# Kernel tuning notes

Measured on AMD Instinct MI355X. Metric: run time of the kernel, lower is better.

Reference implementation:

```python
import jax, jax.numpy as jnp
import numpy as np

B, S, D = 4, 2048, 512

def setup_inputs() -> dict:
    key = jax.random.key(0)
    ks = jax.random.split(key, 7)
    # scale weights so unscaled logits stay in a sane softmax range
    w_scale = 0.05
    return {
        "x": jax.random.normal(ks[0], (B, S, D), dtype=jnp.float32),
        "W_q": jax.random.normal(ks[1], (D, D), dtype=jnp.float32) * w_scale,
        "W_k": jax.random.normal(ks[2], (D, D), dtype=jnp.float32) * w_scale,
        "W_v": jax.random.normal(ks[3], (D, D), dtype=jnp.float32) * w_scale,
        "b_q": jax.random.normal(ks[4], (D,), dtype=jnp.float32) * w_scale,
        "b_k": jax.random.normal(ks[5], (D,), dtype=jnp.float32) * w_scale,
        "b_v": jax.random.normal(ks[6], (D,), dtype=jnp.float32) * w_scale,
    }

def reference(x, W_q, W_k, W_v, b_q, b_k, b_v):
    # QKV projections: [B,S,D] @ [D,D] + [D]
    q = jnp.einsum('bsd,de->bse', x, W_q) + b_q
    k = jnp.einsum('bsd,de->bse', x, W_k) + b_k
    v = jnp.einsum('bsd,de->bse', x, W_v) + b_v
    # unscaled attention scores [B,S,S]
    scores = jnp.einsum('bqd,bkd->bqk', q, k)
    attn = jax.nn.softmax(scores, axis=-1)
    # weighted sum of values [B,S,D]
    return jnp.einsum('bqk,bkd->bqd', attn, v)
```

## Files before the change

### kernel.cpp

```cpp
#include <hip/hip_runtime.h>
#include <hip/hip_bf16.h>
#include <hip/hip_fp16.h>

#define BB 4
#define SS 2048
#define DD 512

typedef short s16x8 __attribute__((ext_vector_type(8)));
typedef short s16x4 __attribute__((ext_vector_type(4)));
typedef float f32x4 __attribute__((ext_vector_type(4)));
typedef _Float16 f16x8 __attribute__((ext_vector_type(8)));

__device__ __forceinline__ short f2h(float f) {
    const _Float16 h = (_Float16)f;
    union { _Float16 h; short s; } u; u.h = h; return u.s;
}
__device__ __forceinline__ float h2f(short s) {
    union { short s; _Float16 h; } u; u.s = s; return (float)u.h;
}
__device__ __forceinline__ f16x8 as_h(s16x8 v) {
    union { s16x8 s; f16x8 h; } u; u.s = v; return u.h;
}

__device__ __forceinline__ void gload_lds16(const void* g, void* l) {
    __builtin_amdgcn_global_load_lds(
        (const __attribute__((address_space(1))) void*)g,
        (__attribute__((address_space(3))) void*)l, 16, 0, 0);
}

#define SB0 __builtin_amdgcn_sched_barrier(0)
#define LGKM0 asm volatile("s_waitcnt lgkmcnt(0)" ::: "memory")
#define VM0   asm volatile("s_waitcnt vmcnt(0)" ::: "memory")

__global__ __launch_bounds__(512, 2) void qkt256(
    const short* __restrict__ qf, const short* __restrict__ kf,
    short* __restrict__ outS, int nwg)
{
    __shared__ short lds[65536];

    const int tid = threadIdx.x;
    const int wave = tid >> 6, lane = tid & 63;
    const int flat = blockIdx.x + 8 * blockIdx.y + 64 * blockIdx.z;
    const int w = (flat & 7) * (nwg >> 3) + (flat >> 3);
    const int bm = ((w >> 3) & 7) * 256, bn = (w & 7) * 256;
    const long z = w >> 6;
    qf += z * (long)SS * DD; kf += z * (long)SS * DD;
    outS += z * (long)SS * SS;

    const int wm = (wave >> 2) * 128, wn = (wave & 3) * 64;
    const int lrow = lane & 15, lk16 = (lane >> 4) * 16;

    f32x4 acc[8][4] = {};

    auto base = [&](int buf, int arr) -> short* { return &lds[(buf * 2 + arr) * 8192]; };
    auto issue = [&](int buf, int arr, int k0) {
#pragma unroll
        for (int h = 0; h < 2; h++) {
            const int Lb = (h << 13) + (tid << 4);
            const int Ls = Lb ^ (((Lb >> 7) & 3) << 4);
            const int row = Ls >> 6, elem = (Ls & 63) >> 1;
            const short* s = arr ? kf : qf;
            const int rb = arr ? bn : bm;
            gload_lds16(s + (size_t)(rb + row) * DD + k0 + elem,
                        (char*)base(buf, arr) + Lb);
        }
    };
    auto rd = [&](int buf, int arr, int row) -> s16x8 {
        const int L = (row << 6) + lk16;
        const int Ls = L ^ (((L >> 7) & 3) << 4);
        return *(const s16x8*)((const char*)base(buf, arr) + Ls);
    };

#define QK_TILE(T, CUR, PREF)                                                    \
  {                                                                              \
    s16x8 a[8], b[4];                                                            \
    _Pragma("unroll")                                                            \
    for (int m = 0; m < 8; m++) a[m] = rd(CUR, 0, wm + m * 16 + lrow);           \
    _Pragma("unroll")                                                            \
    for (int n = 0; n < 4; n++) b[n] = rd(CUR, 1, wn + n * 16 + lrow);           \
    if (PREF) { issue((CUR) ^ 1, 1, ((T) + 1) * 32); SB0;                        \
                issue((CUR) ^ 1, 0, ((T) + 1) * 32); }                           \
    LGKM0; SB0;                                                                  \
    __builtin_amdgcn_s_setprio(1);                                               \
    _Pragma("unroll")                                                            \
    for (int m = 0; m < 8; m++) {                                                \
      _Pragma("unroll")                                                          \
      for (int n = 0; n < 4; n++)                                                \
        acc[m][n] = __builtin_amdgcn_mfma_f32_16x16x32_f16(                      \
            as_h(a[m]), as_h(b[n]), acc[m][n], 0, 0, 0);                         \
    }                                                                            \
    __builtin_amdgcn_s_setprio(0);                                               \
    if (PREF) { VM0; SB0; }                                                      \
    __builtin_amdgcn_s_barrier();                                                \
  }

    issue(0, 1, 0); issue(0, 0, 0);
    VM0;
    __builtin_amdgcn_s_barrier();

    for (int t = 0; t < 16; t += 2) {
        QK_TILE(t,     0, 1);
        QK_TILE(t + 1, 1, (t + 1) < 15);
    }
#undef QK_TILE

    __syncthreads();
    short* ebuf = &lds[0];
#pragma unroll
    for (int m = 0; m < 8; m++) {
#pragma unroll
        for (int n = 0; n < 4; n++) {
#pragma unroll
            for (int j = 0; j < 4; j++) {
                const int rl = wm + m * 16 + (lane >> 4) * 4 + j;
                const int cl = wn + n * 16 + lrow;
                const int pcb = (cl >> 3) ^ ((rl & 3) << 1);
                ebuf[rl * 256 + pcb * 8 + (cl & 7)] =
                    (short)__float2int_rn(acc[m][n][j] * 128.0f);
            }
        }
    }
    __syncthreads();
#pragma unroll
    for (int it = 0; it < 16; it++) {
        const int u = it * 512 + tid;
        const int R = u >> 5, cb = u & 31;
        const int pcb = cb ^ ((R & 3) << 1);
        const s16x8 val = *(const s16x8*)&ebuf[R * 256 + pcb * 8];
        *(s16x8*)&outS[(size_t)(bm + R) * SS + bn + cb * 8] = val;
    }
}

__global__ __launch_bounds__(256, 3) void proj_all(
    const short* __restrict__ xh, const short* __restrict__ xl,
    const short* __restrict__ wt,
    const float* __restrict__ bq, const float* __restrict__ bk,
    const float* __restrict__ bv,
    short* __restrict__ qfp, short* __restrict__ kfp, short* __restrict__ vt)
{
    __shared__ short lds[24576];

    const int tid = threadIdx.x;
    const int wave = tid >> 6, lane = tid & 63;
    const int flat = blockIdx.x + 12 * blockIdx.y;
    const int w = (flat & 7) * 96 + (flat >> 3);
    const int bxi = w % 12, byi = w / 12;
    const int wsel = bxi >> 2;
    const int bnl = (bxi & 3) * 128;
    const int bm = byi * 128;
    const bool lo = (wsel < 2);
    const short* B0 = wt + (size_t)wsel * DD * DD;
    const float* bias = (wsel == 0) ? bq : (wsel == 1) ? bk : bv;

    f32x4 acc[4][4] = {};
    const int wm = (wave >> 1) * 64, wn = (wave & 1) * 64;
    const int lrow = lane & 15, lk16 = (lane >> 4) * 16;

    auto base = [&](int buf, int arr) -> short* { return &lds[(buf * 3 + arr) * 4096]; };
    auto issue = [&](int buf, int arr, int k0) {
#pragma unroll
        for (int h = 0; h < 2; h++) {
            const int Lb = (h << 12) + (tid << 4);
            const int Ls = Lb ^ (((Lb >> 7) & 3) << 4);
            const int row = Ls >> 6, elem = (Ls & 63) >> 1;
            const short* s = (arr == 0) ? xh : (arr == 1) ? xl : B0;
            const int rb = (arr < 2) ? bm : bnl;
            gload_lds16(s + (size_t)(rb + row) * DD + k0 + elem,
                        (char*)base(buf, arr) + Lb);
        }
    };
    auto rd = [&](int buf, int arr, int row) -> s16x8 {
        const int L = (row << 6) + lk16;
        const int Ls = L ^ (((L >> 7) & 3) << 4);
        return *(const s16x8*)((const char*)base(buf, arr) + Ls);
    };

#define PJ_TILE(T, CUR, PREF)                                                    \
  {                                                                              \
    s16x8 ah[4], al[4], b[4];                                                    \
    _Pragma("unroll")                                                            \
    for (int m = 0; m < 4; m++) ah[m] = rd(CUR, 0, wm + m * 16 + lrow);          \
    if (lo) {                                                                    \
      _Pragma("unroll")                                                          \
      for (int m = 0; m < 4; m++) al[m] = rd(CUR, 1, wm + m * 16 + lrow);        \
    }                                                                            \
    _Pragma("unroll")                                                            \
    for (int n = 0; n < 4; n++) b[n] = rd(CUR, 2, wn + n * 16 + lrow);           \
    if (PREF) {                                                                  \
      issue((CUR) ^ 1, 2, ((T) + 1) * 32); SB0;                                  \
      issue((CUR) ^ 1, 0, ((T) + 1) * 32);                                       \
      if (lo) issue((CUR) ^ 1, 1, ((T) + 1) * 32);                               \
    }                                                                            \
    LGKM0; SB0;                                                                  \
    __builtin_amdgcn_s_setprio(1);                                               \
    _Pragma("unroll")                                                            \
    for (int m = 0; m < 4; m++) {                                                \
      _Pragma("unroll")                                                          \
      for (int n = 0; n < 4; n++) {                                              \
        acc[m][n] = __builtin_amdgcn_mfma_f32_16x16x32_f16(                      \
            as_h(ah[m]), as_h(b[n]), acc[m][n], 0, 0, 0);                        \
        if (lo)                                                                  \
          acc[m][n] = __builtin_amdgcn_mfma_f32_16x16x32_f16(                    \
              as_h(al[m]), as_h(b[n]), acc[m][n], 0, 0, 0);                      \
      }                                                                          \
    }                                                                            \
    __builtin_amdgcn_s_setprio(0);                                               \
    if (PREF) { VM0; SB0; }                                                      \
    __builtin_amdgcn_s_barrier();                                                \
  }

    issue(0, 2, 0); issue(0, 0, 0);
    if (lo) issue(0, 1, 0);
    VM0;
    __builtin_amdgcn_s_barrier();

    for (int t = 0; t < 16; t += 2) {
        PJ_TILE(t,     0, 1);
        PJ_TILE(t + 1, 1, (t + 1) < 15);
    }
#undef PJ_TILE

    __syncthreads();
    short* cbuf = &lds[0];
#pragma unroll
    for (int m = 0; m < 4; m++) {
#pragma unroll
        for (int n = 0; n < 4; n++) {
#pragma unroll
            for (int j = 0; j < 4; j++) {
                const int rl = wm + m * 16 + (lane >> 4) * 4 + j;
                const int cl = wn + n * 16 + lrow;
                const float v = acc[m][n][j] + bias[bnl + cl];
                if (wsel < 2)
                    cbuf[rl * 128 + (cl ^ ((rl & 7) << 3))] = f2h(v);
                else
                    cbuf[cl * 128 + (rl ^ ((cl & 7) << 3))] = f2h(v);
            }
        }
    }
    __syncthreads();
    if (wsel < 2) {
        short* outp = wsel ? kfp : qfp;
#pragma unroll
        for (int it = 0; it < 8; it++) {
            const int u = it * 256 + tid;
            const int r = u >> 4, c8 = (u & 15) * 8;
            const s16x8 val = *(const s16x8*)&cbuf[r * 128 + (c8 ^ ((r & 7) << 3))];
            *(s16x8*)&outp[(size_t)(bm + r) * DD + bnl + c8] = val;
        }
    } else {
        const int b = bm >> 11, s0 = bm & 2047;
#pragma unroll
        for (int it = 0; it < 8; it++) {
            const int idx = it * 256 + tid;
            const int dd = idx >> 4, c8 = (idx & 15) * 8;
            const s16x8 val = *(const s16x8*)&cbuf[dd * 128 + (c8 ^ ((dd & 7) << 3))];
            *(s16x8*)&vt[((size_t)b << 20) + ((size_t)(bnl + dd) << 11) + s0 + c8] = val;
        }
    }
}

__global__ __launch_bounds__(256, 3) void pv_gemm(
    const short* __restrict__ P, const short* __restrict__ vt,
    float* __restrict__ out, int nwg)
{
    __shared__ short As[2][64 * 64];
    __shared__ short Bs[2][128 * 64];

    const int tid = threadIdx.x;
    const int wave = tid >> 6, lane = tid & 63;
    const int flat = blockIdx.x + 4 * blockIdx.y + 128 * blockIdx.z;
    const int w = (flat & 7) * (nwg >> 3) + (flat >> 3);
    const int bm = ((w >> 2) & 31) * 64, bn = (w & 3) * 128;
    const long z = w >> 7;
    P += z * (long)SS * SS;
    vt += z << 20;
    out += z * (long)SS * DD;

    f32x4 acc[2][4] = {};
    const int wm = (wave >> 1) * 32, wn = (wave & 1) * 64;
    const int lrow = lane & 15, lk = (lane >> 4) * 8;

    auto swz = [](int L) { return L ^ (((L >> 7) & 7) << 4); };
    auto issueA = [&](int buf, int k0) {
#pragma unroll
        for (int h = 0; h < 2; h++) {
            const int L = (h << 12) + (tid << 4);
            const int Ls = swz(L);
            const int row = Ls >> 7, col = (Ls & 127) >> 1;
            gload_lds16(P + (size_t)(bm + row) * SS + k0 + col, (char*)&As[buf][0] + L);
        }
    };
    auto issueB = [&](int buf, int k0) {
#pragma unroll
        for (int h = 0; h < 4; h++) {
            const int L = (h << 12) + (tid << 4);
            const int Ls = swz(L);
            const int row = Ls >> 7, col = (Ls & 127) >> 1;
            gload_lds16(vt + ((size_t)(bn + row) << 11) + k0 + col, (char*)&Bs[buf][0] + L);
        }
    };

#define PV_TILE(T, CUR, PREF)                                                    \
  {                                                                              \
    s16x8 a[2][2], b[2][4];                                                      \
    _Pragma("unroll")                                                            \
    for (int kx = 0; kx < 2; kx++) {                                             \
      _Pragma("unroll")                                                          \
      for (int m = 0; m < 2; m++)                                                \
        a[kx][m] = *(const s16x8*)((const char*)&As[CUR][0] +                    \
                   swz(((wm + m * 16 + lrow) * 64 + kx * 32 + lk) * 2));         \
      _Pragma("unroll")                                                          \
      for (int n = 0; n < 4; n++)                                                \
        b[kx][n] = *(const s16x8*)((const char*)&Bs[CUR][0] +                    \
                   swz(((wn + n * 16 + lrow) * 64 + kx * 32 + lk) * 2));         \
    }                                                                            \
    if (PREF) { issueB((CUR) ^ 1, ((T) + 1) * 64); SB0;                          \
                issueA((CUR) ^ 1, ((T) + 1) * 64); }                             \
    LGKM0; SB0;                                                                  \
    __builtin_amdgcn_s_setprio(1);                                               \
    _Pragma("unroll")                                                            \
    for (int kx = 0; kx < 2; kx++) {                                             \
      _Pragma("unroll")                                                          \
      for (int m = 0; m < 2; m++) {                                              \
        _Pragma("unroll")                                                        \
        for (int n = 0; n < 4; n++)                                              \
          acc[m][n] = __builtin_amdgcn_mfma_f32_16x16x32_f16(                    \
              as_h(a[kx][m]), as_h(b[kx][n]), acc[m][n], 0, 0, 0);               \
      }                                                                          \
    }                                                                            \
    __builtin_amdgcn_s_setprio(0);                                               \
    if (PREF) { VM0; SB0; }                                                      \
    __builtin_amdgcn_s_barrier();                                                \
  }

    issueB(0, 0); issueA(0, 0);
    VM0;
    __builtin_amdgcn_s_barrier();

    for (int t = 0; t < 32; t += 2) {
        PV_TILE(t,     0, 1);
        PV_TILE(t + 1, 1, (t + 1) < 31);
    }
#undef PV_TILE

#pragma unroll
    for (int m = 0; m < 2; m++) {
#pragma unroll
        for (int n = 0; n < 4; n++) {
#pragma unroll
            for (int j = 0; j < 4; j++) {
                const int row = bm + wm + m * 16 + (lane >> 4) * 4 + j;
                const int col = bn + wn + n * 16 + lrow;
                out[(size_t)row * DD + col] = acc[m][n][j];
            }
        }
    }
}

__global__ __launch_bounds__(256) void cast_all(
    const float* __restrict__ x,
    const float* __restrict__ wq, const float* __restrict__ wk,
    const float* __restrict__ wv,
    short* __restrict__ xh, short* __restrict__ xl,
    short* __restrict__ wt)
{
    const int bid = blockIdx.x;
    if (bid < 4096) {
        const int i = bid * 256 + threadIdx.x;
        const float4 v = ((const float4*)x)[i];
        const float vv[4] = {v.x, v.y, v.z, v.w};
        s16x4 h, l;
#pragma unroll
        for (int j = 0; j < 4; j++) {
            const short hh = f2h(vv[j]);
            h[j] = hh;
            l[j] = f2h(vv[j] - h2f(hh));
        }
        ((s16x4*)xh)[i] = h;
        ((s16x4*)xl)[i] = l;
    } else {
        const int t = (bid - 4096) * 256 + threadIdx.x;
        const int w = t >> 18;
        const int r = t & 262143;
        const float* src = (w == 0) ? wq : ((w == 1) ? wk : wv);
        const float v = src[r];
        const int k = r >> 9, n = r & 511;
        wt[((size_t)w << 18) + ((size_t)n << 9) + k] = f2h(v);
    }
}

__global__ __launch_bounds__(256) void softmax_rows(
    const short* __restrict__ S, short* __restrict__ P)
{
    const int row = blockIdx.x;
    const long z = blockIdx.y;
    const short* s = S + z * (long)SS * SS + (long)row * SS;
    short* p = P + z * (long)SS * SS + (long)row * SS;
    const int tid = threadIdx.x;

    const s16x8 raw = ((const s16x8*)s)[tid];
    float v[8];
#pragma unroll
    for (int j = 0; j < 8; j++) v[j] = (float)(int)raw[j] * 0.0078125f;

    float m = v[0];
#pragma unroll
    for (int j = 1; j < 8; j++) m = fmaxf(m, v[j]);
#pragma unroll
    for (int off = 32; off >= 1; off >>= 1) m = fmaxf(m, __shfl_xor(m, off));
    __shared__ float redm[4], reds[4];
    if ((tid & 63) == 0) redm[tid >> 6] = m;
    __syncthreads();
    m = fmaxf(fmaxf(redm[0], redm[1]), fmaxf(redm[2], redm[3]));

    float e[8], sum = 0.f;
#pragma unroll
    for (int j = 0; j < 8; j++) { e[j] = __expf(v[j] - m); sum += e[j]; }
#pragma unroll
    for (int off = 32; off >= 1; off >>= 1) sum += __shfl_xor(sum, off);
    if ((tid & 63) == 0) reds[tid >> 6] = sum;
    __syncthreads();
    sum = reds[0] + reds[1] + reds[2] + reds[3];
    const float inv = 1.0f / sum;

    s16x8 o;
#pragma unroll
    for (int j = 0; j < 8; j++) o[j] = f2h(e[j] * inv);
    ((s16x8*)p)[tid] = o;
}

extern "C" void kernel_launch(void* const* d_in, const int* in_sizes, int n_in,
                              void* d_out, int out_size, void* d_ws, size_t ws_size,
                              hipStream_t stream)
{
    const float* x  = (const float*)d_in[0];
    const float* Wq = (const float*)d_in[1];
    const float* Wk = (const float*)d_in[2];
    const float* Wv = (const float*)d_in[3];
    const float* bq = (const float*)d_in[4];
    const float* bk = (const float*)d_in[5];
    const float* bv = (const float*)d_in[6];
    float* out = (float*)d_out;

    const size_t MK = (size_t)BB * SS * DD;
    char* ws = (char*)d_ws;
    short* xh  = (short*)ws; ws += MK * 2;
    short* xl  = (short*)ws; ws += MK * 2;
    short* wt  = (short*)ws; ws += 3ull * DD * DD * 2;
    short* qfp = (short*)ws; ws += MK * 2;
    short* kfp = (short*)ws; ws += MK * 2;
    short* vt  = (short*)ws; ws += MK * 2;
    const size_t fixed = (size_t)(ws - (char*)d_ws);

    int g = 4;
    while (g > 0 && fixed + (size_t)g * ((size_t)SS * SS * 2 + (size_t)SS * SS * 2) > ws_size)
        g >>= 1;
    if (g == 0) return;
    short* sc = (short*)ws;
    short* P  = (short*)(ws + (size_t)g * SS * SS * 2);

    cast_all<<<dim3(7168), 256, 0, stream>>>(x, Wq, Wk, Wv, xh, xl, wt);
    proj_all<<<dim3(12, 64), 256, 0, stream>>>(xh, xl, wt, bq, bk, bv,
                                               qfp, kfp, vt);

    for (int b0 = 0; b0 < BB; b0 += g) {
        const int gg = (b0 + g <= BB) ? g : (BB - b0);
        qkt256<<<dim3(8, 8, gg), 512, 0, stream>>>(
            qfp + (size_t)b0 * SS * DD, kfp + (size_t)b0 * SS * DD, sc, 64 * gg);
        softmax_rows<<<dim3(SS, gg), 256, 0, stream>>>(sc, P);
        pv_gemm<<<dim3(4, 32, gg), 256, 0, stream>>>(
            P, vt + ((size_t)b0 << 20), out + (size_t)b0 * SS * DD, 128 * gg);
    }
}
```

Before: 107.8 us.

## Fuse softmax into QK^T epilogue row stats and PV operand load

Removes the standalone softmax kernel. The QK^T kernel now emits a partial row max and exp-sum for each 256-column tile. The PV kernel combines these into a final max and inverse sum, then applies exp and normalization while staging score tiles into LDS through registers instead of async global-to-LDS loads. This drops one full read and write pass over the S×S score matrix and one kernel launch. In exchange, PV redoes the exp for every element, and its A operand loses the direct-to-LDS async load path.

```diff
diff --git a/kernel.cpp b/kernel.cpp
--- a/kernel.cpp
+++ b/kernel.cpp
@@ -34,7 +34,7 @@
 
 __global__ __launch_bounds__(512, 2) void qkt256(
     const short* __restrict__ qf, const short* __restrict__ kf,
-    short* __restrict__ outS, int nwg)
+    short* __restrict__ outS, float2* __restrict__ rowstat, int nwg)
 {
     __shared__ short lds[65536];
 
@@ -46,6 +46,7 @@
     const long z = w >> 6;
     qf += z * (long)SS * DD; kf += z * (long)SS * DD;
     outS += z * (long)SS * SS;
+    rowstat += z * 8 * SS;
 
     const int wm = (wave >> 2) * 128, wn = (wave & 3) * 64;
     const int lrow = lane & 15, lk16 = (lane >> 4) * 16;
@@ -128,6 +129,21 @@
         const int pcb = cb ^ ((R & 3) << 1);
         const s16x8 val = *(const s16x8*)&ebuf[R * 256 + pcb * 8];
         *(s16x8*)&outS[(size_t)(bm + R) * SS + bn + cb * 8] = val;
+        float vf[8], vmax = -3e38f;
+#pragma unroll
+        for (int j = 0; j < 8; j++) {
+            vf[j] = (float)(int)val[j] * 0.0078125f;
+            vmax = fmaxf(vmax, vf[j]);
+        }
+#pragma unroll
+        for (int off = 1; off <= 16; off <<= 1) vmax = fmaxf(vmax, __shfl_xor(vmax, off));
+        float se = 0.f;
+#pragma unroll
+        for (int j = 0; j < 8; j++) se += __expf(vf[j] - vmax);
+#pragma unroll
+        for (int off = 1; off <= 16; off <<= 1) se += __shfl_xor(se, off);
+        if ((tid & 31) == 0)
+            rowstat[(size_t)(bn >> 8) * SS + bm + R] = make_float2(vmax, se);
     }
 }
 
@@ -260,12 +276,13 @@
     }
 }
 
-__global__ __launch_bounds__(256, 3) void pv_gemm(
-    const short* __restrict__ P, const short* __restrict__ vt,
-    float* __restrict__ out, int nwg)
+__global__ __launch_bounds__(256, 3) void pv_fused(
+    const short* __restrict__ S, const short* __restrict__ vt,
+    const float2* __restrict__ rowstat, float* __restrict__ out, int nwg)
 {
     __shared__ short As[2][64 * 64];
     __shared__ short Bs[2][128 * 64];
+    __shared__ float mrowL[64], sinvL[64];
 
     const int tid = threadIdx.x;
     const int wave = tid >> 6, lane = tid & 63;
@@ -273,24 +290,36 @@
     const int w = (flat & 7) * (nwg >> 3) + (flat >> 3);
     const int bm = ((w >> 2) & 31) * 64, bn = (w & 3) * 128;
     const long z = w >> 7;
-    P += z * (long)SS * SS;
+    S += z * (long)SS * SS;
     vt += z << 20;
     out += z * (long)SS * DD;
+    rowstat += z * 8 * SS;
+
+    if (tid < 64) {
+        float2 v[8];
+        float m = -3e38f;
+#pragma unroll
+        for (int b = 0; b < 8; b++) {
+            v[b] = rowstat[(size_t)b * SS + bm + tid];
+            m = fmaxf(m, v[b].x);
+        }
+        float s = 0.f;
+#pragma unroll
+        for (int b = 0; b < 8; b++) s += v[b].y * __expf(v[b].x - m);
+        mrowL[tid] = m;
+        sinvL[tid] = 1.0f / s;
+    }
+    __syncthreads();
+
+    const int ar0 = tid >> 3, ac0 = (tid & 7) * 8;
+    const float m0 = mrowL[ar0], i0 = sinvL[ar0];
+    const float m1 = mrowL[32 + ar0], i1 = sinvL[32 + ar0];
 
     f32x4 acc[2][4] = {};
     const int wm = (wave >> 1) * 32, wn = (wave & 1) * 64;
     const int lrow = lane & 15, lk = (lane >> 4) * 8;
 
     auto swz = [](int L) { return L ^ (((L >> 7) & 7) << 4); };
-    auto issueA = [&](int buf, int k0) {
-#pragma unroll
-        for (int h = 0; h < 2; h++) {
-            const int L = (h << 12) + (tid << 4);
-            const int Ls = swz(L);
-            const int row = Ls >> 7, col = (Ls & 127) >> 1;
-            gload_lds16(P + (size_t)(bm + row) * SS + k0 + col, (char*)&As[buf][0] + L);
-        }
-    };
     auto issueB = [&](int buf, int k0) {
 #pragma unroll
         for (int h = 0; h < 4; h++) {
@@ -300,6 +329,18 @@
             gload_lds16(vt + ((size_t)(bn + row) << 11) + k0 + col, (char*)&Bs[buf][0] + L);
         }
     };
+    auto loadA = [&](int k0, s16x8& r0, s16x8& r1) {
+        r0 = *(const s16x8*)&S[(size_t)(bm + ar0) * SS + k0 + ac0];
+        r1 = *(const s16x8*)&S[(size_t)(bm + 32 + ar0) * SS + k0 + ac0];
+    };
+    auto expWrite = [&](int buf, s16x8 r, int rowbase, float mm, float ii) {
+        s16x8 o;
+#pragma unroll
+        for (int j = 0; j < 8; j++)
+            o[j] = f2h(__expf((float)(int)r[j] * 0.0078125f - mm) * ii);
+        const int L = ((rowbase + ar0) << 7) + ((tid & 7) << 4);
+        *(s16x8*)((char*)&As[buf][0] + swz(L)) = o;
+    };
 
 #define PV_TILE(T, CUR, PREF)                                                    \
   {                                                                              \
@@ -315,8 +356,9 @@
         b[kx][n] = *(const s16x8*)((const char*)&Bs[CUR][0] +                    \
                    swz(((wn + n * 16 + lrow) * 64 + kx * 32 + lk) * 2));         \
     }                                                                            \
+    s16x8 n0, n1;                                                                \
     if (PREF) { issueB((CUR) ^ 1, ((T) + 1) * 64); SB0;                          \
-                issueA((CUR) ^ 1, ((T) + 1) * 64); }                             \
+                loadA(((T) + 1) * 64, n0, n1); }                                 \
     LGKM0; SB0;                                                                  \
     __builtin_amdgcn_s_setprio(1);                                               \
     _Pragma("unroll")                                                            \
@@ -330,12 +372,24 @@
       }                                                                          \
     }                                                                            \
     __builtin_amdgcn_s_setprio(0);                                               \
-    if (PREF) { VM0; SB0; }                                                      \
+    if (PREF) {                                                                  \
+      VM0; SB0;                                                                  \
+      expWrite((CUR) ^ 1, n0, 0, m0, i0);                                        \
+      expWrite((CUR) ^ 1, n1, 32, m1, i1);                                       \
+      LGKM0; SB0;                                                                \
+    }                                                                            \
     __builtin_amdgcn_s_barrier();                                                \
   }
 
-    issueB(0, 0); issueA(0, 0);
-    VM0;
+    issueB(0, 0);
+    {
+        s16x8 p0, p1;
+        loadA(0, p0, p1);
+        VM0;
+        expWrite(0, p0, 0, m0, i0);
+        expWrite(0, p1, 32, m1, i1);
+        LGKM0;
+    }
     __builtin_amdgcn_s_barrier();
 
     for (int t = 0; t < 32; t += 2) {
@@ -390,46 +444,6 @@
     }
 }
 
-__global__ __launch_bounds__(256) void softmax_rows(
-    const short* __restrict__ S, short* __restrict__ P)
-{
-    const int row = blockIdx.x;
-    const long z = blockIdx.y;
-    const short* s = S + z * (long)SS * SS + (long)row * SS;
-    short* p = P + z * (long)SS * SS + (long)row * SS;
-    const int tid = threadIdx.x;
-
-    const s16x8 raw = ((const s16x8*)s)[tid];
-    float v[8];
-#pragma unroll
-    for (int j = 0; j < 8; j++) v[j] = (float)(int)raw[j] * 0.0078125f;
-
-    float m = v[0];
-#pragma unroll
-    for (int j = 1; j < 8; j++) m = fmaxf(m, v[j]);
-#pragma unroll
-    for (int off = 32; off >= 1; off >>= 1) m = fmaxf(m, __shfl_xor(m, off));
-    __shared__ float redm[4], reds[4];
-    if ((tid & 63) == 0) redm[tid >> 6] = m;
-    __syncthreads();
-    m = fmaxf(fmaxf(redm[0], redm[1]), fmaxf(redm[2], redm[3]));
-
-    float e[8], sum = 0.f;
-#pragma unroll
-    for (int j = 0; j < 8; j++) { e[j] = __expf(v[j] - m); sum += e[j]; }
-#pragma unroll
-    for (int off = 32; off >= 1; off >>= 1) sum += __shfl_xor(sum, off);
-    if ((tid & 63) == 0) reds[tid >> 6] = sum;
-    __syncthreads();
-    sum = reds[0] + reds[1] + reds[2] + reds[3];
-    const float inv = 1.0f / sum;
-
-    s16x8 o;
-#pragma unroll
-    for (int j = 0; j < 8; j++) o[j] = f2h(e[j] * inv);
-    ((s16x8*)p)[tid] = o;
-}
-
 extern "C" void kernel_launch(void* const* d_in, const int* in_sizes, int n_in,
                               void* d_out, int out_size, void* d_ws, size_t ws_size,
                               hipStream_t stream)
@@ -451,14 +465,14 @@
     short* qfp = (short*)ws; ws += MK * 2;
     short* kfp = (short*)ws; ws += MK * 2;
     short* vt  = (short*)ws; ws += MK * 2;
+    float2* rowstat = (float2*)ws; ws += (size_t)BB * 8 * SS * sizeof(float2);
     const size_t fixed = (size_t)(ws - (char*)d_ws);
 
     int g = 4;
-    while (g > 0 && fixed + (size_t)g * ((size_t)SS * SS * 2 + (size_t)SS * SS * 2) > ws_size)
+    while (g > 0 && fixed + (size_t)g * ((size_t)SS * SS * 2) > ws_size)
         g >>= 1;
     if (g == 0) return;
     short* sc = (short*)ws;
-    short* P  = (short*)(ws + (size_t)g * SS * SS * 2);
 
     cast_all<<<dim3(7168), 256, 0, stream>>>(x, Wq, Wk, Wv, xh, xl, wt);
     proj_all<<<dim3(12, 64), 256, 0, stream>>>(xh, xl, wt, bq, bk, bv,
@@ -467,9 +481,10 @@
     for (int b0 = 0; b0 < BB; b0 += g) {
         const int gg = (b0 + g <= BB) ? g : (BB - b0);
         qkt256<<<dim3(8, 8, gg), 512, 0, stream>>>(
-            qfp + (size_t)b0 * SS * DD, kfp + (size_t)b0 * SS * DD, sc, 64 * gg);
-        softmax_rows<<<dim3(SS, gg), 256, 0, stream>>>(sc, P);
-        pv_gemm<<<dim3(4, 32, gg), 256, 0, stream>>>(
-            P, vt + ((size_t)b0 << 20), out + (size_t)b0 * SS * DD, 128 * gg);
-    }
-}
+            qfp + (size_t)b0 * SS * DD, kfp + (size_t)b0 * SS * DD,
+            sc, rowstat + (size_t)b0 * 8 * SS, 64 * gg);
+        pv_fused<<<dim3(4, 32, gg), 256, 0, stream>>>(
+            sc, vt + ((size_t)b0 << 20),
+            rowstat + (size_t)b0 * 8 * SS, out + (size_t)b0 * SS * DD, 128 * gg);
+    }
+}
```

New measurement: 111.6 us. +3.6%, slower.
